# Kernel optimization log

Hardware: AMD Instinct MI355X
Metric: run time of the kernel (lower is better)

The kernel has to match this reference:

```python
import jax, jax.numpy as jnp
import numpy as np

DIM = 512
HEADS = 8
DIM_HEAD = 64
INNER = HEADS * DIM_HEAD
EPS = 1e-5


def setup_inputs() -> dict:
    key = jax.random.key(0)
    ks = jax.random.split(key, 8)
    x = jax.random.normal(ks[0], (4, 2048, DIM), dtype=jnp.float32)
    gamma = jnp.ones((DIM,), jnp.float32)
    beta = jnp.zeros((DIM,), jnp.float32)
    Wq = jax.random.normal(ks[1], (DIM, INNER), jnp.float32) / np.sqrt(DIM)
    Wkv = jax.random.normal(ks[2], (DIM, 2 * INNER), jnp.float32) / np.sqrt(DIM)
    mix_pre = jax.random.normal(ks[3], (HEADS, HEADS), jnp.float32)
    mix_post = jax.random.normal(ks[4], (HEADS, HEADS), jnp.float32)
    Wout = jax.random.normal(ks[5], (INNER, DIM), jnp.float32) / np.sqrt(INNER)
    bout = jnp.zeros((DIM,), jnp.float32)
    return {"x": x, "gamma": gamma, "beta": beta, "Wq": Wq, "Wkv": Wkv,
            "mix_pre": mix_pre, "mix_post": mix_post, "Wout": Wout, "bout": bout}


def reference(x, gamma, beta, Wq, Wkv, mix_pre, mix_post, Wout, bout):
    b, n, _ = x.shape
    scale = DIM_HEAD ** -0.5
    # LayerNorm
    mu = jnp.mean(x, axis=-1, keepdims=True)
    var = jnp.mean(jnp.square(x - mu), axis=-1, keepdims=True)
    xn = (x - mu) / jnp.sqrt(var + EPS) * gamma + beta
    # projections -> (b, h, n, d)
    q = (xn @ Wq).reshape(b, n, HEADS, DIM_HEAD).transpose(0, 2, 1, 3)
    kv = xn @ Wkv
    k, v = jnp.split(kv, 2, axis=-1)
    k = k.reshape(b, n, HEADS, DIM_HEAD).transpose(0, 2, 1, 3)
    v = v.reshape(b, n, HEADS, DIM_HEAD).transpose(0, 2, 1, 3)
    # talking-heads attention
    dots = jnp.einsum('bhid,bhjd->bhij', q, k) * scale
    dots = jnp.einsum('bhij,hg->bgij', dots, mix_pre)
    attn = jax.nn.softmax(dots, axis=-1)
    attn = jnp.einsum('bhij,hg->bgij', attn, mix_post)
    out = jnp.einsum('bhij,bhjd->bhid', attn, v)  # (b,h,n,d)
    out = out.transpose(0, 2, 1, 3).reshape(b, n, INNER)
    return out @ Wout + bout
```

## Files before the change

### kernel.cpp

```cpp
#include <hip/hip_runtime.h>

using short8  = short     __attribute__((ext_vector_type(8)));
using half4   = _Float16  __attribute__((ext_vector_type(4)));
using float4_ = float     __attribute__((ext_vector_type(4)));

__device__ __forceinline__ unsigned short f2bf(float f) {
  union { float f; unsigned u; } v; v.f = f;
  unsigned r = v.u + 0x7fffu + ((v.u >> 16) & 1u);
  return (unsigned short)(r >> 16);
}

__global__ __launch_bounds__(256, 4) void ln_kernel(
    const float* __restrict__ x, const float* __restrict__ gamma,
    const float* __restrict__ beta, unsigned short* __restrict__ xn) {
  int w = threadIdx.x >> 6, lane = threadIdx.x & 63;
  int row = blockIdx.x * 4 + w;
  const float4_* xr = (const float4_*)(x + row * 512);
  float4_ v0 = xr[lane * 2], v1 = xr[lane * 2 + 1];
  float s = 0.f, ss = 0.f;
#pragma unroll
  for (int e = 0; e < 4; ++e) { s += v0[e] + v1[e]; ss += v0[e]*v0[e] + v1[e]*v1[e]; }
#pragma unroll
  for (int off = 1; off < 64; off <<= 1) { s += __shfl_xor(s, off); ss += __shfl_xor(ss, off); }
  float mu = s * (1.f/512.f);
  float var = ss * (1.f/512.f) - mu*mu;
  float rs = rsqrtf(var + 1e-5f);
  const float4_* gp = (const float4_*)gamma;
  const float4_* bp = (const float4_*)beta;
  float4_ g0 = gp[lane*2], g1 = gp[lane*2+1], b0 = bp[lane*2], b1 = bp[lane*2+1];
  short8 pk;
#pragma unroll
  for (int e = 0; e < 4; ++e) {
    pk[e]   = (short)f2bf((v0[e]-mu)*rs*g0[e] + b0[e]);
    pk[e+4] = (short)f2bf((v1[e]-mu)*rs*g1[e] + b1[e]);
  }
  *(short8*)&xn[row*512 + lane*8] = pk;
}

__global__ __launch_bounds__(256, 4) void wconv(
    const float* __restrict__ Wq, const float* __restrict__ Wkv,
    const float* __restrict__ Wout, unsigned short* __restrict__ wt,
    unsigned short* __restrict__ wot) {
  int t = blockIdx.x * 256 + threadIdx.x;
  if (t < 786432) {
    int k = t / 1536, n = t % 1536;
    float v = (n < 512) ? Wq[k*512 + n] * 0.125f : Wkv[k*1024 + (n - 512)];
    wt[n*512 + k] = f2bf(v);
  } else {
    int t2 = t - 786432;
    int k = t2 >> 9, n = t2 & 511;
    wot[n*512 + k] = f2bf(Wout[k*512 + n]);
  }
}

__global__ __launch_bounds__(256, 2) void qkv_gemm(
    const unsigned short* __restrict__ A, const unsigned short* __restrict__ Bt,
    unsigned short* __restrict__ Qs, unsigned short* __restrict__ Kb,
    _Float16* __restrict__ Vt) {
  __shared__ unsigned short lA[128*32];
  __shared__ unsigned short lB[128*32];
  int bid = blockIdx.x;
  int tm = bid & 63, tn = bid >> 6;
  int m0 = tm * 128, n0 = tn * 128;
  int tid = threadIdx.x, lane = tid & 63, w = tid >> 6;
  int lrow = lane & 15, lgrp = lane >> 4;
  int wr = w >> 1, wc = w & 1;
  int r0 = tid >> 2, c0 = tid & 3;
  float4_ acc[4][4];
#pragma unroll
  for (int mi = 0; mi < 4; ++mi)
#pragma unroll
    for (int ni = 0; ni < 4; ++ni) acc[mi][ni] = (float4_){0.f,0.f,0.f,0.f};

  for (int k0 = 0; k0 < 512; k0 += 32) {
    short8 a0 = *(const short8*)&A[(m0 + r0)*512 + k0 + c0*8];
    short8 a1 = *(const short8*)&A[(m0 + 64 + r0)*512 + k0 + c0*8];
    short8 b0 = *(const short8*)&Bt[(n0 + r0)*512 + k0 + c0*8];
    short8 b1 = *(const short8*)&Bt[(n0 + 64 + r0)*512 + k0 + c0*8];
    __syncthreads();
    *(short8*)&lA[tid*8] = a0; *(short8*)&lA[(tid+256)*8] = a1;
    *(short8*)&lB[tid*8] = b0; *(short8*)&lB[(tid+256)*8] = b1;
    __syncthreads();
    short8 af[4], bfr[4];
#pragma unroll
    for (int mi = 0; mi < 4; ++mi) af[mi]  = *(const short8*)&lA[(wr*64 + mi*16 + lrow)*32 + lgrp*8];
#pragma unroll
    for (int ni = 0; ni < 4; ++ni) bfr[ni] = *(const short8*)&lB[(wc*64 + ni*16 + lrow)*32 + lgrp*8];
#pragma unroll
    for (int mi = 0; mi < 4; ++mi)
#pragma unroll
      for (int ni = 0; ni < 4; ++ni)
        acc[mi][ni] = __builtin_amdgcn_mfma_f32_16x16x32_bf16(af[mi], bfr[ni], acc[mi][ni], 0, 0, 0);
  }
#pragma unroll
  for (int mi = 0; mi < 4; ++mi) {
#pragma unroll
    for (int ni = 0; ni < 4; ++ni) {
      int col = n0 + wc*64 + ni*16 + lrow;
#pragma unroll
      for (int r = 0; r < 4; ++r) {
        int row = m0 + wr*64 + mi*16 + lgrp*4 + r;
        float v = acc[mi][ni][r];
        int b = row >> 11, i = row & 2047;
        if (col < 1024) {
          unsigned short* dst = (col < 512) ? Qs : Kb;
          int c = col & 511;
          dst[(((b<<3) + (c>>6))*2048 + i)*64 + (c & 63)] = f2bf(v);
        } else {
          int c = col - 1024;
          Vt[(((b<<3) + (c>>6))*64 + (c & 63))*2048 + i] = (_Float16)v;
        }
      }
    }
  }
}

__global__ __launch_bounds__(256, 1) void attn_kernel(
    const unsigned short* __restrict__ Qs, const unsigned short* __restrict__ Kb,
    const _Float16* __restrict__ Vt, const float* __restrict__ mixp,
    const float* __restrict__ mixq, unsigned short* __restrict__ AO) {
  int bid = blockIdx.x;
  int xcd = bid & 7;
  int b = xcd >> 1;
  int it = ((xcd & 1) << 6) | (bid >> 3);
  int i0 = it << 4;
  int tid = threadIdx.x, w = tid >> 6, lane = tid & 63;
  int lrow = lane & 15, lgrp = lane >> 4;

  __shared__ float Lm[4][8][16];
  __shared__ float Ll[4][8][16];
  __shared__ float Ob[8][64][16];

  short8 qf[8][2];
#pragma unroll
  for (int h = 0; h < 8; ++h) {
    int base = (((b<<3)+h)*2048 + i0 + lrow)*64 + lgrp*8;
#pragma unroll
    for (int t = 0; t < 2; ++t) qf[h][t] = *(const short8*)&Qs[base + t*32];
  }

  float m_[8], l_[8];
#pragma unroll
  for (int g = 0; g < 8; ++g) { m_[g] = -1e30f; l_[g] = 0.f; }

  for (int jt = w; jt < 128; jt += 4) {
    int j0 = jt << 4;
    short8 kfr[8][2];
#pragma unroll
    for (int h = 0; h < 8; ++h) {
      int base = (((b<<3)+h)*2048 + j0 + lrow)*64 + lgrp*8;
      kfr[h][0] = *(const short8*)&Kb[base];
      kfr[h][1] = *(const short8*)&Kb[base + 32];
    }
    float4_ S[8];
#pragma unroll
    for (int h = 0; h < 8; ++h) {
      float4_ z = {0.f,0.f,0.f,0.f};
      z = __builtin_amdgcn_mfma_f32_16x16x32_bf16(kfr[h][0], qf[h][0], z, 0, 0, 0);
      S[h] = __builtin_amdgcn_mfma_f32_16x16x32_bf16(kfr[h][1], qf[h][1], z, 0, 0, 0);
    }
#pragma unroll
    for (int g = 0; g < 8; ++g) {
      float4_ sg = S[0] * mixp[g];
#pragma unroll
      for (int h = 1; h < 8; ++h) sg += S[h] * mixp[h*8 + g];
      float tm = fmaxf(fmaxf(sg[0], sg[1]), fmaxf(sg[2], sg[3]));
      float mn = fmaxf(m_[g], tm);
      l_[g] = l_[g]*__expf(m_[g]-mn) + __expf(sg[0]-mn) + __expf(sg[1]-mn)
            + __expf(sg[2]-mn) + __expf(sg[3]-mn);
      m_[g] = mn;
    }
  }
#pragma unroll
  for (int g = 0; g < 8; ++g) {
#pragma unroll
    for (int off = 16; off < 64; off <<= 1) {
      float om = __shfl_xor(m_[g], off);
      float ol = __shfl_xor(l_[g], off);
      float mn = fmaxf(m_[g], om);
      l_[g] = l_[g]*__expf(m_[g]-mn) + ol*__expf(om-mn);
      m_[g] = mn;
    }
  }
  if (lgrp == 0) {
#pragma unroll
    for (int g = 0; g < 8; ++g) { Lm[w][g][lrow] = m_[g]; Ll[w][g][lrow] = l_[g]; }
  }
  __syncthreads();
  float mm[8];
#pragma unroll
  for (int g = 0; g < 8; ++g) {
    float M = Lm[0][g][lrow], L = Ll[0][g][lrow];
#pragma unroll
    for (int wv = 1; wv < 4; ++wv) {
      float om = Lm[wv][g][lrow], ol = Ll[wv][g][lrow];
      float mn = fmaxf(M, om);
      L = L*__expf(M-mn) + ol*__expf(om-mn);
      M = mn;
    }
    mm[g] = M + __logf(L);
  }

  float4_ ot[8][4];
#pragma unroll
  for (int g = 0; g < 8; ++g)
#pragma unroll
    for (int dt = 0; dt < 4; ++dt) ot[g][dt] = (float4_){0.f,0.f,0.f,0.f};

  for (int jt = w; jt < 128; jt += 4) {
    int j0 = jt << 4;
    short8 kfr[8][2];
#pragma unroll
    for (int h = 0; h < 8; ++h) {
      int base = (((b<<3)+h)*2048 + j0 + lrow)*64 + lgrp*8;
      kfr[h][0] = *(const short8*)&Kb[base];
      kfr[h][1] = *(const short8*)&Kb[base + 32];
    }
    float4_ S[8];
#pragma unroll
    for (int h = 0; h < 8; ++h) {
      float4_ z = {0.f,0.f,0.f,0.f};
      z = __builtin_amdgcn_mfma_f32_16x16x32_bf16(kfr[h][0], qf[h][0], z, 0, 0, 0);
      S[h] = __builtin_amdgcn_mfma_f32_16x16x32_bf16(kfr[h][1], qf[h][1], z, 0, 0, 0);
    }
    half4 vf[8][4];
#pragma unroll
    for (int g = 0; g < 8; ++g) {
      int vbase = ((((b<<3)+g)<<6) + lrow)*2048 + j0 + lgrp*4;
#pragma unroll
      for (int dt = 0; dt < 4; ++dt) vf[g][dt] = *(const half4*)&Vt[vbase + dt*16*2048];
    }
    float4_ P[8];
#pragma unroll
    for (int g = 0; g < 8; ++g) {
      float4_ sg = S[0] * mixp[g];
#pragma unroll
      for (int h = 1; h < 8; ++h) sg += S[h] * mixp[h*8 + g];
      float4_ p;
      p[0] = __expf(sg[0] - mm[g]); p[1] = __expf(sg[1] - mm[g]);
      p[2] = __expf(sg[2] - mm[g]); p[3] = __expf(sg[3] - mm[g]);
      P[g] = p;
    }
#pragma unroll
    for (int g = 0; g < 8; ++g) {
      float4_ ag = P[0] * mixq[g];
#pragma unroll
      for (int h = 1; h < 8; ++h) ag += P[h] * mixq[h*8 + g];
      half4 pb;
      pb[0] = (_Float16)ag[0]; pb[1] = (_Float16)ag[1];
      pb[2] = (_Float16)ag[2]; pb[3] = (_Float16)ag[3];
#pragma unroll
      for (int dt = 0; dt < 4; ++dt)
        ot[g][dt] = __builtin_amdgcn_mfma_f32_16x16x16f16(vf[g][dt], pb, ot[g][dt], 0, 0, 0);
    }
  }

#pragma unroll
  for (int wv = 0; wv < 4; ++wv) {
    if (w == wv) {
#pragma unroll
      for (int g = 0; g < 8; ++g)
#pragma unroll
        for (int dt = 0; dt < 4; ++dt)
#pragma unroll
          for (int r = 0; r < 4; ++r) {
            int d = dt*16 + lgrp*4 + r;
            if (wv == 0) Ob[g][d][lrow] = ot[g][dt][r];
            else         Ob[g][d][lrow] += ot[g][dt][r];
          }
    }
    __syncthreads();
  }
  int i = tid >> 4;
  int gd0 = (tid & 15) * 32;
  unsigned short* dst = &AO[(b*2048 + i0 + i)*512 + gd0];
  const float* ob = (const float*)Ob;
#pragma unroll
  for (int c = 0; c < 32; c += 8) {
    short8 pk;
#pragma unroll
    for (int e = 0; e < 8; ++e) pk[e] = (short)f2bf(ob[(gd0 + c + e)*16 + i]);
    *(short8*)&dst[c] = pk;
  }
}

__global__ __launch_bounds__(256, 2) void out_gemm(
    const unsigned short* __restrict__ A, const unsigned short* __restrict__ Bt,
    const float* __restrict__ bout, float* __restrict__ out) {
  __shared__ unsigned short lA[128*32];
  __shared__ unsigned short lB[128*32];
  int bid = blockIdx.x;
  int tm = bid & 63, tn = bid >> 6;
  int m0 = tm * 128, n0 = tn * 128;
  int tid = threadIdx.x, lane = tid & 63, w = tid >> 6;
  int lrow = lane & 15, lgrp = lane >> 4;
  int wr = w >> 1, wc = w & 1;
  int r0 = tid >> 2, c0 = tid & 3;
  float4_ acc[4][4];
#pragma unroll
  for (int mi = 0; mi < 4; ++mi)
#pragma unroll
    for (int ni = 0; ni < 4; ++ni) acc[mi][ni] = (float4_){0.f,0.f,0.f,0.f};

  for (int k0 = 0; k0 < 512; k0 += 32) {
    short8 a0 = *(const short8*)&A[(m0 + r0)*512 + k0 + c0*8];
    short8 a1 = *(const short8*)&A[(m0 + 64 + r0)*512 + k0 + c0*8];
    short8 b0 = *(const short8*)&Bt[(n0 + r0)*512 + k0 + c0*8];
    short8 b1 = *(const short8*)&Bt[(n0 + 64 + r0)*512 + k0 + c0*8];
    __syncthreads();
    *(short8*)&lA[tid*8] = a0; *(short8*)&lA[(tid+256)*8] = a1;
    *(short8*)&lB[tid*8] = b0; *(short8*)&lB[(tid+256)*8] = b1;
    __syncthreads();
    short8 af[4], bfr[4];
#pragma unroll
    for (int mi = 0; mi < 4; ++mi) af[mi]  = *(const short8*)&lA[(wr*64 + mi*16 + lrow)*32 + lgrp*8];
#pragma unroll
    for (int ni = 0; ni < 4; ++ni) bfr[ni] = *(const short8*)&lB[(wc*64 + ni*16 + lrow)*32 + lgrp*8];
#pragma unroll
    for (int mi = 0; mi < 4; ++mi)
#pragma unroll
      for (int ni = 0; ni < 4; ++ni)
        acc[mi][ni] = __builtin_amdgcn_mfma_f32_16x16x32_bf16(af[mi], bfr[ni], acc[mi][ni], 0, 0, 0);
  }
#pragma unroll
  for (int mi = 0; mi < 4; ++mi)
#pragma unroll
    for (int ni = 0; ni < 4; ++ni) {
      int col = n0 + wc*64 + ni*16 + lrow;
      float bb = bout[col];
#pragma unroll
      for (int r = 0; r < 4; ++r) {
        int row = m0 + wr*64 + mi*16 + lgrp*4 + r;
        out[row*512 + col] = acc[mi][ni][r] + bb;
      }
    }
}

extern "C" void kernel_launch(void* const* d_in, const int* in_sizes, int n_in,
                              void* d_out, int out_size, void* d_ws, size_t ws_size,
                              hipStream_t stream) {
  (void)in_sizes; (void)n_in; (void)out_size; (void)ws_size;
  const float* x     = (const float*)d_in[0];
  const float* gamma = (const float*)d_in[1];
  const float* beta  = (const float*)d_in[2];
  const float* Wq    = (const float*)d_in[3];
  const float* Wkv   = (const float*)d_in[4];
  const float* mixp  = (const float*)d_in[5];
  const float* mixq  = (const float*)d_in[6];
  const float* Wout  = (const float*)d_in[7];
  const float* bout  = (const float*)d_in[8];
  float* out = (float*)d_out;

  unsigned short* xn  = (unsigned short*)d_ws;
  unsigned short* wt  = xn  + 4194304;
  unsigned short* wot = wt  + 786432;
  unsigned short* Qs  = wot + 262144;
  unsigned short* Kb  = Qs  + 4194304;
  _Float16*       Vt  = (_Float16*)(Kb + 4194304);
  unsigned short* AO  = (unsigned short*)(Vt + 4194304);

  ln_kernel<<<2048, 256, 0, stream>>>(x, gamma, beta, xn);
  wconv<<<4096, 256, 0, stream>>>(Wq, Wkv, Wout, wt, wot);
  qkv_gemm<<<768, 256, 0, stream>>>(xn, wt, Qs, Kb, Vt);
  attn_kernel<<<512, 256, 0, stream>>>(Qs, Kb, Vt, mixp, mixq, AO);
  out_gemm<<<256, 256, 0, stream>>>(AO, wot, bout, out);
}
```

Measured before the change: 610.0 us.

## Split talking-heads attention into stats, merge and output kernels

The single attention kernel becomes three kernels. A stats pass splits the key range in two across blocks, a small kernel merges the partial max/sum, and an output pass splits the post-mix output heads in half across blocks. This gives 1024 blocks instead of 512 with higher occupancy, and the mixing coefficients are held in scalar registers. The post-softmax mix now runs in packed fp16, and Q is staged through LDS. In exchange, the output pass recomputes all eight QK head products for each half of the heads, adds an extra launch and intermediate buffers, and does the mix arithmetic at lower precision.

```diff
diff --git a/kernel.cpp b/kernel.cpp
--- a/kernel.cpp
+++ b/kernel.cpp
@@ -1,13 +1,21 @@
 #include <hip/hip_runtime.h>
 
 using short8  = short     __attribute__((ext_vector_type(8)));
+using half2v  = _Float16  __attribute__((ext_vector_type(2)));
 using half4   = _Float16  __attribute__((ext_vector_type(4)));
+using float2_ = float     __attribute__((ext_vector_type(2)));
 using float4_ = float     __attribute__((ext_vector_type(4)));
 
 __device__ __forceinline__ unsigned short f2bf(float f) {
   union { float f; unsigned u; } v; v.f = f;
   unsigned r = v.u + 0x7fffu + ((v.u >> 16) & 1u);
   return (unsigned short)(r >> 16);
+}
+__device__ __forceinline__ float sgprf(float x) {
+  return __int_as_float(__builtin_amdgcn_readfirstlane(__float_as_int(x)));
+}
+__device__ __forceinline__ half2v pkrtz(float a, float b) {
+  return __builtin_bit_cast(half2v, __builtin_amdgcn_cvt_pkrtz(a, b));
 }
 
 __global__ __launch_bounds__(256, 4) void ln_kernel(
@@ -39,17 +47,25 @@
 
 __global__ __launch_bounds__(256, 4) void wconv(
     const float* __restrict__ Wq, const float* __restrict__ Wkv,
-    const float* __restrict__ Wout, unsigned short* __restrict__ wt,
-    unsigned short* __restrict__ wot) {
+    const float* __restrict__ Wout, const float* __restrict__ mixq,
+    unsigned short* __restrict__ wt, unsigned short* __restrict__ wot,
+    unsigned int* __restrict__ mqp) {
   int t = blockIdx.x * 256 + threadIdx.x;
   if (t < 786432) {
     int k = t / 1536, n = t % 1536;
     float v = (n < 512) ? Wq[k*512 + n] * 0.125f : Wkv[k*1024 + (n - 512)];
     wt[n*512 + k] = f2bf(v);
-  } else {
+  } else if (t < 1048576) {
     int t2 = t - 786432;
     int k = t2 >> 9, n = t2 & 511;
     wot[n*512 + k] = f2bf(Wout[k*512 + n]);
+  } else if (t < 1048608) {
+    int idx = t - 1048576;
+    int gp = idx >> 2, p = idx & 3;
+    _Float16 lo = (_Float16)mixq[gp*8 + 2*p];
+    _Float16 hi = (_Float16)mixq[gp*8 + 2*p + 1];
+    unsigned short lb = *(unsigned short*)&lo, hb = *(unsigned short*)&hi;
+    mqp[idx] = (unsigned)lb | ((unsigned)hb << 16);
   }
 }
 
@@ -115,59 +131,76 @@
   }
 }
 
-__global__ __launch_bounds__(256, 1) void attn_kernel(
+__device__ __forceinline__ void stage_q(const unsigned short* __restrict__ Qs,
+                                        unsigned short* qlds, int b, int i0, int tid) {
+#pragma unroll
+  for (int q = 0; q < 4; ++q) {
+    int idx = q*256 + tid;
+    int h = idx >> 7, i = (idx >> 3) & 15, c = idx & 7;
+    short8 v = *(const short8*)&Qs[(((b<<3)+h)*2048 + i0 + i)*64 + c*8];
+    *(short8*)&qlds[((h*8 + c)*16 + i)*8] = v;
+  }
+}
+
+__global__ __launch_bounds__(256, 4) void attn1(
     const unsigned short* __restrict__ Qs, const unsigned short* __restrict__ Kb,
-    const _Float16* __restrict__ Vt, const float* __restrict__ mixp,
-    const float* __restrict__ mixq, unsigned short* __restrict__ AO) {
+    const float* __restrict__ mixp, float* __restrict__ ml) {
+  __shared__ unsigned short qlds[8192];
+  __shared__ float Lm[4][8][16], Ll[4][8][16];
   int bid = blockIdx.x;
-  int xcd = bid & 7;
-  int b = xcd >> 1;
-  int it = ((xcd & 1) << 6) | (bid >> 3);
+  int xcd = bid & 7, b = xcd >> 1, jh = xcd & 1, it = bid >> 3;
   int i0 = it << 4;
   int tid = threadIdx.x, w = tid >> 6, lane = tid & 63;
   int lrow = lane & 15, lgrp = lane >> 4;
 
-  __shared__ float Lm[4][8][16];
-  __shared__ float Ll[4][8][16];
-  __shared__ float Ob[8][64][16];
-
-  short8 qf[8][2];
-#pragma unroll
-  for (int h = 0; h < 8; ++h) {
-    int base = (((b<<3)+h)*2048 + i0 + lrow)*64 + lgrp*8;
-#pragma unroll
-    for (int t = 0; t < 2; ++t) qf[h][t] = *(const short8*)&Qs[base + t*32];
-  }
+  float mp[64];
+#pragma unroll
+  for (int k = 0; k < 64; ++k) mp[k] = sgprf(mixp[k]);
+
+  stage_q(Qs, qlds, b, i0, tid);
+  __syncthreads();
 
   float m_[8], l_[8];
 #pragma unroll
   for (int g = 0; g < 8; ++g) { m_[g] = -1e30f; l_[g] = 0.f; }
 
-  for (int jt = w; jt < 128; jt += 4) {
+  for (int t = 0; t < 16; ++t) {
+    int jt = (jh << 6) + w + (t << 2);
     int j0 = jt << 4;
-    short8 kfr[8][2];
-#pragma unroll
-    for (int h = 0; h < 8; ++h) {
-      int base = (((b<<3)+h)*2048 + j0 + lrow)*64 + lgrp*8;
-      kfr[h][0] = *(const short8*)&Kb[base];
-      kfr[h][1] = *(const short8*)&Kb[base + 32];
-    }
     float4_ S[8];
 #pragma unroll
-    for (int h = 0; h < 8; ++h) {
-      float4_ z = {0.f,0.f,0.f,0.f};
-      z = __builtin_amdgcn_mfma_f32_16x16x32_bf16(kfr[h][0], qf[h][0], z, 0, 0, 0);
-      S[h] = __builtin_amdgcn_mfma_f32_16x16x32_bf16(kfr[h][1], qf[h][1], z, 0, 0, 0);
+    for (int hb = 0; hb < 2; ++hb) {
+      short8 kf[4][2];
+#pragma unroll
+      for (int hh = 0; hh < 4; ++hh) {
+        const unsigned short* kp = &Kb[(((b<<3)+hb*4+hh)*2048 + j0 + lrow)*64 + lgrp*8];
+        kf[hh][0] = *(const short8*)kp;
+        kf[hh][1] = *(const short8*)(kp + 32);
+      }
+#pragma unroll
+      for (int hh = 0; hh < 4; ++hh) {
+        int h = hb*4 + hh;
+        short8 q0 = *(const short8*)&qlds[((h*8 + lgrp)*16 + lrow)*8];
+        short8 q1 = *(const short8*)&qlds[((h*8 + lgrp + 4)*16 + lrow)*8];
+        float4_ z = {0.f,0.f,0.f,0.f};
+        z = __builtin_amdgcn_mfma_f32_16x16x32_bf16(kf[hh][0], q0, z, 0, 0, 0);
+        S[h] = __builtin_amdgcn_mfma_f32_16x16x32_bf16(kf[hh][1], q1, z, 0, 0, 0);
+      }
     }
 #pragma unroll
     for (int g = 0; g < 8; ++g) {
-      float4_ sg = S[0] * mixp[g];
-#pragma unroll
-      for (int h = 1; h < 8; ++h) sg += S[h] * mixp[h*8 + g];
-      float tm = fmaxf(fmaxf(sg[0], sg[1]), fmaxf(sg[2], sg[3]));
+      float2_ sa = (float2_){S[0][0], S[0][1]} * mp[g];
+      float2_ sb = (float2_){S[0][2], S[0][3]} * mp[g];
+#pragma unroll
+      for (int h = 1; h < 8; ++h) {
+        float m = mp[h*8 + g];
+        sa += (float2_){S[h][0], S[h][1]} * m;
+        sb += (float2_){S[h][2], S[h][3]} * m;
+      }
+      float tm = fmaxf(fmaxf(sa[0], sa[1]), fmaxf(sb[0], sb[1]));
       float mn = fmaxf(m_[g], tm);
-      l_[g] = l_[g]*__expf(m_[g]-mn) + __expf(sg[0]-mn) + __expf(sg[1]-mn)
-            + __expf(sg[2]-mn) + __expf(sg[3]-mn);
+      l_[g] = l_[g]*__expf(m_[g]-mn) + __expf(sa[0]-mn) + __expf(sa[1]-mn)
+            + __expf(sb[0]-mn) + __expf(sb[1]-mn);
       m_[g] = mn;
     }
   }
@@ -187,79 +220,139 @@
     for (int g = 0; g < 8; ++g) { Lm[w][g][lrow] = m_[g]; Ll[w][g][lrow] = l_[g]; }
   }
   __syncthreads();
-  float mm[8];
-#pragma unroll
-  for (int g = 0; g < 8; ++g) {
-    float M = Lm[0][g][lrow], L = Ll[0][g][lrow];
-#pragma unroll
-    for (int wv = 1; wv < 4; ++wv) {
-      float om = Lm[wv][g][lrow], ol = Ll[wv][g][lrow];
-      float mn = fmaxf(M, om);
-      L = L*__expf(M-mn) + ol*__expf(om-mn);
-      M = mn;
-    }
-    mm[g] = M + __logf(L);
-  }
-
-  float4_ ot[8][4];
-#pragma unroll
-  for (int g = 0; g < 8; ++g)
+  if (w == 0 && lgrp == 0) {
+    int gi = b*2048 + i0 + lrow;
+#pragma unroll
+    for (int g = 0; g < 8; ++g) {
+      float M = Lm[0][g][lrow], L = Ll[0][g][lrow];
+#pragma unroll
+      for (int wv = 1; wv < 4; ++wv) {
+        float om = Lm[wv][g][lrow], ol = Ll[wv][g][lrow];
+        float mn = fmaxf(M, om);
+        L = L*__expf(M-mn) + ol*__expf(om-mn); M = mn;
+      }
+      ml[((jh*8192 + gi)*8 + g)*2]     = M;
+      ml[((jh*8192 + gi)*8 + g)*2 + 1] = L;
+    }
+  }
+}
+
+__global__ __launch_bounds__(256, 8) void attn1m(const float* __restrict__ ml,
+                                                 float* __restrict__ mm) {
+  int idx = blockIdx.x*256 + threadIdx.x;
+  float m0 = ml[idx*2], l0 = ml[idx*2+1];
+  float m1 = ml[(65536+idx)*2], l1 = ml[(65536+idx)*2+1];
+  float M = fmaxf(m0, m1);
+  float L = l0*__expf(m0-M) + l1*__expf(m1-M);
+  mm[idx] = M + __logf(L);
+}
+
+__global__ __launch_bounds__(256, 3) void attn2(
+    const unsigned short* __restrict__ Qs, const unsigned short* __restrict__ Kb,
+    const _Float16* __restrict__ Vt, const float* __restrict__ mixp,
+    const unsigned int* __restrict__ mqp, const float* __restrict__ mm,
+    unsigned short* __restrict__ AO) {
+  __shared__ unsigned short qlds[8192];
+  __shared__ float Ob[4][64][16];
+  int bid = blockIdx.x;
+  int xcd = bid & 7, b = xcd >> 1, gh = xcd & 1, it = bid >> 3;
+  int i0 = it << 4;
+  int tid = threadIdx.x, w = tid >> 6, lane = tid & 63;
+  int lrow = lane & 15, lgrp = lane >> 4;
+
+  float mp[64];
+#pragma unroll
+  for (int k = 0; k < 64; ++k) mp[k] = sgprf(mixp[k]);
+  half2v mq2[8][2];
+#pragma unroll
+  for (int gp = 0; gp < 8; ++gp)
+#pragma unroll
+    for (int p = 0; p < 2; ++p) {
+      unsigned u = mqp[gp*4 + gh*2 + p];
+      mq2[gp][p] = __builtin_bit_cast(half2v, u);
+    }
+
+  stage_q(Qs, qlds, b, i0, tid);
+  float mmr[8];
+  int gi = b*2048 + i0 + lrow;
+#pragma unroll
+  for (int g = 0; g < 8; ++g) mmr[g] = mm[gi*8 + g];
+  __syncthreads();
+
+  float4_ ot[4][4];
+#pragma unroll
+  for (int g = 0; g < 4; ++g)
 #pragma unroll
     for (int dt = 0; dt < 4; ++dt) ot[g][dt] = (float4_){0.f,0.f,0.f,0.f};
 
-  for (int jt = w; jt < 128; jt += 4) {
+  for (int t = 0; t < 32; ++t) {
+    int jt = w + (t << 2);
     int j0 = jt << 4;
-    short8 kfr[8][2];
-#pragma unroll
-    for (int h = 0; h < 8; ++h) {
-      int base = (((b<<3)+h)*2048 + j0 + lrow)*64 + lgrp*8;
-      kfr[h][0] = *(const short8*)&Kb[base];
-      kfr[h][1] = *(const short8*)&Kb[base + 32];
-    }
     float4_ S[8];
 #pragma unroll
-    for (int h = 0; h < 8; ++h) {
-      float4_ z = {0.f,0.f,0.f,0.f};
-      z = __builtin_amdgcn_mfma_f32_16x16x32_bf16(kfr[h][0], qf[h][0], z, 0, 0, 0);
-      S[h] = __builtin_amdgcn_mfma_f32_16x16x32_bf16(kfr[h][1], qf[h][1], z, 0, 0, 0);
-    }
-    half4 vf[8][4];
+    for (int hb = 0; hb < 4; ++hb) {
+      short8 kf[2][2];
+#pragma unroll
+      for (int hh = 0; hh < 2; ++hh) {
+        const unsigned short* kp = &Kb[(((b<<3)+hb*2+hh)*2048 + j0 + lrow)*64 + lgrp*8];
+        kf[hh][0] = *(const short8*)kp;
+        kf[hh][1] = *(const short8*)(kp + 32);
+      }
+#pragma unroll
+      for (int hh = 0; hh < 2; ++hh) {
+        int h = hb*2 + hh;
+        short8 q0 = *(const short8*)&qlds[((h*8 + lgrp)*16 + lrow)*8];
+        short8 q1 = *(const short8*)&qlds[((h*8 + lgrp + 4)*16 + lrow)*8];
+        float4_ z = {0.f,0.f,0.f,0.f};
+        z = __builtin_amdgcn_mfma_f32_16x16x32_bf16(kf[hh][0], q0, z, 0, 0, 0);
+        S[h] = __builtin_amdgcn_mfma_f32_16x16x32_bf16(kf[hh][1], q1, z, 0, 0, 0);
+      }
+    }
+    half2v agv[4][2];
+#pragma unroll
+    for (int r = 0; r < 4; ++r) { agv[r][0] = (half2v)0; agv[r][1] = (half2v)0; }
 #pragma unroll
     for (int g = 0; g < 8; ++g) {
-      int vbase = ((((b<<3)+g)<<6) + lrow)*2048 + j0 + lgrp*4;
-#pragma unroll
-      for (int dt = 0; dt < 4; ++dt) vf[g][dt] = *(const half4*)&Vt[vbase + dt*16*2048];
-    }
-    float4_ P[8];
-#pragma unroll
-    for (int g = 0; g < 8; ++g) {
-      float4_ sg = S[0] * mixp[g];
-#pragma unroll
-      for (int h = 1; h < 8; ++h) sg += S[h] * mixp[h*8 + g];
-      float4_ p;
-      p[0] = __expf(sg[0] - mm[g]); p[1] = __expf(sg[1] - mm[g]);
-      p[2] = __expf(sg[2] - mm[g]); p[3] = __expf(sg[3] - mm[g]);
-      P[g] = p;
-    }
-#pragma unroll
-    for (int g = 0; g < 8; ++g) {
-      float4_ ag = P[0] * mixq[g];
-#pragma unroll
-      for (int h = 1; h < 8; ++h) ag += P[h] * mixq[h*8 + g];
-      half4 pb;
-      pb[0] = (_Float16)ag[0]; pb[1] = (_Float16)ag[1];
-      pb[2] = (_Float16)ag[2]; pb[3] = (_Float16)ag[3];
-#pragma unroll
-      for (int dt = 0; dt < 4; ++dt)
-        ot[g][dt] = __builtin_amdgcn_mfma_f32_16x16x16f16(vf[g][dt], pb, ot[g][dt], 0, 0, 0);
-    }
-  }
-
+      float2_ sa = (float2_){S[0][0], S[0][1]} * mp[g];
+      float2_ sb = (float2_){S[0][2], S[0][3]} * mp[g];
+#pragma unroll
+      for (int h = 1; h < 8; ++h) {
+        float m = mp[h*8 + g];
+        sa += (float2_){S[h][0], S[h][1]} * m;
+        sb += (float2_){S[h][2], S[h][3]} * m;
+      }
+      float p0 = __expf(sa[0]-mmr[g]), p1 = __expf(sa[1]-mmr[g]);
+      float p2 = __expf(sb[0]-mmr[g]), p3 = __expf(sb[1]-mmr[g]);
+      half2v d0 = pkrtz(p0, p0);
+      half2v d1 = pkrtz(p1, p1);
+      half2v d2 = pkrtz(p2, p2);
+      half2v d3 = pkrtz(p3, p3);
+      agv[0][0] += d0*mq2[g][0]; agv[0][1] += d0*mq2[g][1];
+      agv[1][0] += d1*mq2[g][0]; agv[1][1] += d1*mq2[g][1];
+      agv[2][0] += d2*mq2[g][0]; agv[2][1] += d2*mq2[g][1];
+      agv[3][0] += d3*mq2[g][0]; agv[3][1] += d3*mq2[g][1];
+    }
+    half4 pb[4];
+#pragma unroll
+    for (int g = 0; g < 4; ++g) {
+#pragma unroll
+      for (int r = 0; r < 4; ++r) pb[g][r] = agv[r][g >> 1][g & 1];
+    }
+#pragma unroll
+    for (int g = 0; g < 4; ++g) {
+      const _Float16* vb = &Vt[(((b<<3) + gh*4 + g)*64 + lrow)*2048 + j0 + lgrp*4];
+#pragma unroll
+      for (int dt = 0; dt < 4; ++dt) {
+        half4 vf = *(const half4*)&vb[dt*16*2048];
+        ot[g][dt] = __builtin_amdgcn_mfma_f32_16x16x16f16(vf, pb[g], ot[g][dt], 0, 0, 0);
+      }
+    }
+  }
 #pragma unroll
   for (int wv = 0; wv < 4; ++wv) {
     if (w == wv) {
 #pragma unroll
-      for (int g = 0; g < 8; ++g)
+      for (int g = 0; g < 4; ++g)
 #pragma unroll
         for (int dt = 0; dt < 4; ++dt)
 #pragma unroll
@@ -271,17 +364,18 @@
     }
     __syncthreads();
   }
-  int i = tid >> 4;
-  int gd0 = (tid & 15) * 32;
-  unsigned short* dst = &AO[(b*2048 + i0 + i)*512 + gd0];
-  const float* ob = (const float*)Ob;
-#pragma unroll
-  for (int c = 0; c < 32; c += 8) {
-    short8 pk;
-#pragma unroll
-    for (int e = 0; e < 8; ++e) pk[e] = (short)f2bf(ob[(gd0 + c + e)*16 + i]);
-    *(short8*)&dst[c] = pk;
-  }
+  int i = tid >> 4, cc = tid & 15;
+  unsigned short* dst = &AO[(b*2048 + i0 + i)*512 + gh*256 + cc*16];
+  short8 o0, o1;
+#pragma unroll
+  for (int e = 0; e < 8; ++e) {
+    int c = cc*16 + e;
+    o0[e] = (short)f2bf(Ob[c>>6][c&63][i]);
+    int c2 = c + 8;
+    o1[e] = (short)f2bf(Ob[c2>>6][c2&63][i]);
+  }
+  *(short8*)dst = o0;
+  *(short8*)(dst + 8) = o1;
 }
 
 __global__ __launch_bounds__(256, 2) void out_gemm(
@@ -358,10 +452,15 @@
   unsigned short* Kb  = Qs  + 4194304;
   _Float16*       Vt  = (_Float16*)(Kb + 4194304);
   unsigned short* AO  = (unsigned short*)(Vt + 4194304);
+  unsigned int*   mqp = (unsigned int*)(AO + 4194304);
+  float*          ml  = (float*)(mqp + 32);
+  float*          mm  = ml + 262144;
 
   ln_kernel<<<2048, 256, 0, stream>>>(x, gamma, beta, xn);
-  wconv<<<4096, 256, 0, stream>>>(Wq, Wkv, Wout, wt, wot);
+  wconv<<<4097, 256, 0, stream>>>(Wq, Wkv, Wout, mixq, wt, wot, mqp);
   qkv_gemm<<<768, 256, 0, stream>>>(xn, wt, Qs, Kb, Vt);
-  attn_kernel<<<512, 256, 0, stream>>>(Qs, Kb, Vt, mixp, mixq, AO);
+  attn1<<<1024, 256, 0, stream>>>(Qs, Kb, mixp, ml);
+  attn1m<<<256, 256, 0, stream>>>(ml, mm);
+  attn2<<<1024, 256, 0, stream>>>(Qs, Kb, Vt, mixp, mqp, mm, AO);
   out_gemm<<<256, 256, 0, stream>>>(AO, wot, bout, out);
 }
```

Result: slower. 1.038 ms (+70.1%).

## Split attention work per head across waves with LDS exchange for head mixing

Applied to the files above, without the earlier changes.

The attention kernel now uses 512 threads, one wave per head, instead of 4 waves that each handle all 8 heads over a strided slice of key tiles. Each wave computes QK for its own head over every key tile and writes fp16-packed scores to a double-buffered LDS array. After a barrier, every wave reads all heads' scores to apply the pre-softmax mix, and in the second pass the post-softmax mix, using packed half2 arithmetic. K loads are software-pipelined one tile ahead, and the cross-wave Ob reduction and merge of softmax statistics are removed. In exchange there are one or two block barriers per key tile, and scores and probabilities are rounded to fp16 (round-toward-zero) before mixing, which lowers accuracy.

```diff
diff --git a/kernel.cpp b/kernel.cpp
--- a/kernel.cpp
+++ b/kernel.cpp
@@ -1,13 +1,25 @@
 #include <hip/hip_runtime.h>
 
+using short4_ = short     __attribute__((ext_vector_type(4)));
 using short8  = short     __attribute__((ext_vector_type(8)));
+using half2v  = _Float16  __attribute__((ext_vector_type(2)));
 using half4   = _Float16  __attribute__((ext_vector_type(4)));
+using float2_ = float     __attribute__((ext_vector_type(2)));
 using float4_ = float     __attribute__((ext_vector_type(4)));
 
 __device__ __forceinline__ unsigned short f2bf(float f) {
   union { float f; unsigned u; } v; v.f = f;
   unsigned r = v.u + 0x7fffu + ((v.u >> 16) & 1u);
   return (unsigned short)(r >> 16);
+}
+__device__ __forceinline__ float sgprf(float x) {
+  return __int_as_float(__builtin_amdgcn_readfirstlane(__float_as_int(x)));
+}
+__device__ __forceinline__ half2v pkrtz(float a, float b) {
+  return __builtin_bit_cast(half2v, __builtin_amdgcn_cvt_pkrtz(a, b));
+}
+__device__ __forceinline__ void bar_lds() {
+  asm volatile("s_waitcnt lgkmcnt(0)\ns_barrier" ::: "memory");
 }
 
 __global__ __launch_bounds__(256, 4) void ln_kernel(
@@ -39,8 +51,8 @@
 
 __global__ __launch_bounds__(256, 4) void wconv(
     const float* __restrict__ Wq, const float* __restrict__ Wkv,
-    const float* __restrict__ Wout, unsigned short* __restrict__ wt,
-    unsigned short* __restrict__ wot) {
+    const float* __restrict__ Wout,
+    unsigned short* __restrict__ wt, unsigned short* __restrict__ wot) {
   int t = blockIdx.x * 256 + threadIdx.x;
   if (t < 786432) {
     int k = t / 1536, n = t % 1536;
@@ -115,172 +127,149 @@
   }
 }
 
-__global__ __launch_bounds__(256, 1) void attn_kernel(
+__global__ __launch_bounds__(512, 4) void attn_f(
     const unsigned short* __restrict__ Qs, const unsigned short* __restrict__ Kb,
     const _Float16* __restrict__ Vt, const float* __restrict__ mixp,
     const float* __restrict__ mixq, unsigned short* __restrict__ AO) {
+  __shared__ unsigned long long sbuf[2][8][64];
+  __shared__ unsigned long long pbuf[2][8][64];
   int bid = blockIdx.x;
-  int xcd = bid & 7;
-  int b = xcd >> 1;
-  int it = ((xcd & 1) << 6) | (bid >> 3);
+  int b = (bid & 7) >> 1;
+  int it = ((bid >> 3) << 1) | (bid & 1);
   int i0 = it << 4;
   int tid = threadIdx.x, w = tid >> 6, lane = tid & 63;
   int lrow = lane & 15, lgrp = lane >> 4;
-
-  __shared__ float Lm[4][8][16];
-  __shared__ float Ll[4][8][16];
-  __shared__ float Ob[8][64][16];
-
-  short8 qf[8][2];
-#pragma unroll
-  for (int h = 0; h < 8; ++h) {
-    int base = (((b<<3)+h)*2048 + i0 + lrow)*64 + lgrp*8;
-#pragma unroll
-    for (int t = 0; t < 2; ++t) qf[h][t] = *(const short8*)&Qs[base + t*32];
-  }
-
-  float m_[8], l_[8];
-#pragma unroll
-  for (int g = 0; g < 8; ++g) { m_[g] = -1e30f; l_[g] = 0.f; }
-
-  for (int jt = w; jt < 128; jt += 4) {
-    int j0 = jt << 4;
-    short8 kfr[8][2];
+  int bh = (b << 3) + w;
+
+  float mp[8];
+#pragma unroll
+  for (int h = 0; h < 8; ++h) mp[h] = sgprf(mixp[h*8 + w]);
+  unsigned mqs[8];
+#pragma unroll
+  for (int g = 0; g < 8; ++g) {
+    float v = mixq[g*8 + w];
+    half2v h2 = pkrtz(v, v);
+    mqs[g] = (unsigned)__builtin_amdgcn_readfirstlane((int)__builtin_bit_cast(unsigned, h2));
+  }
+
+  const unsigned short* qp = &Qs[(bh*2048 + i0 + lrow)*64 + lgrp*8];
+  short8 qf0 = *(const short8*)qp;
+  short8 qf1 = *(const short8*)(qp + 32);
+
+  const unsigned short* kbase = &Kb[(bh*2048 + lrow)*64 + lgrp*8];
+  const _Float16*       vbase = &Vt[(bh*64 + lrow)*2048 + lgrp*4];
+
+  short8 ka0 = *(const short8*)kbase;
+  short8 ka1 = *(const short8*)(kbase + 32);
+  short8 kb0, kb1;
+
+  float m_ = -1e30f, l_ = 0.f;
+
+  auto p1body = [&](int t, short8& c0, short8& c1, short8& n0, short8& n1) {
+    const unsigned short* kn = kbase + (((t + 1) & 127) << 10);
+    n0 = *(const short8*)kn;
+    n1 = *(const short8*)(kn + 32);
+    float4_ S = {0.f,0.f,0.f,0.f};
+    S = __builtin_amdgcn_mfma_f32_16x16x32_bf16(c0, qf0, S, 0, 0, 0);
+    S = __builtin_amdgcn_mfma_f32_16x16x32_bf16(c1, qf1, S, 0, 0, 0);
+    unsigned lo = __builtin_bit_cast(unsigned, pkrtz(S[0], S[1]));
+    unsigned hi = __builtin_bit_cast(unsigned, pkrtz(S[2], S[3]));
+    sbuf[t & 1][w][lane] = (unsigned long long)lo | ((unsigned long long)hi << 32);
+    bar_lds();
+    float s0 = 0.f, s1 = 0.f, s2 = 0.f, s3 = 0.f;
 #pragma unroll
     for (int h = 0; h < 8; ++h) {
-      int base = (((b<<3)+h)*2048 + j0 + lrow)*64 + lgrp*8;
-      kfr[h][0] = *(const short8*)&Kb[base];
-      kfr[h][1] = *(const short8*)&Kb[base + 32];
-    }
-    float4_ S[8];
+      unsigned long long u = sbuf[t & 1][h][lane];
+      half2v l2 = __builtin_bit_cast(half2v, (unsigned)u);
+      half2v h2 = __builtin_bit_cast(half2v, (unsigned)(u >> 32));
+      s0 = fmaf(mp[h], (float)l2[0], s0);
+      s1 = fmaf(mp[h], (float)l2[1], s1);
+      s2 = fmaf(mp[h], (float)h2[0], s2);
+      s3 = fmaf(mp[h], (float)h2[1], s3);
+    }
+    float tm = fmaxf(fmaxf(s0, s1), fmaxf(s2, s3));
+    float mn = fmaxf(m_, tm);
+    l_ = l_*__expf(m_-mn) + __expf(s0-mn) + __expf(s1-mn) + __expf(s2-mn) + __expf(s3-mn);
+    m_ = mn;
+  };
+  for (int tt = 0; tt < 64; ++tt) {
+    p1body(2*tt,     ka0, ka1, kb0, kb1);
+    p1body(2*tt + 1, kb0, kb1, ka0, ka1);
+  }
+#pragma unroll
+  for (int off = 16; off < 64; off <<= 1) {
+    float om = __shfl_xor(m_, off);
+    float ol = __shfl_xor(l_, off);
+    float mn = fmaxf(m_, om);
+    l_ = l_*__expf(m_-mn) + ol*__expf(om-mn);
+    m_ = mn;
+  }
+  float mm = m_ + __logf(l_);
+
+  float4_ ot0 = {0.f,0.f,0.f,0.f}, ot1 = ot0, ot2 = ot0, ot3 = ot0;
+  auto p2body = [&](int t, short8& c0, short8& c1, short8& n0, short8& n1) {
+    const unsigned short* kn = kbase + (((t + 1) & 127) << 10);
+    n0 = *(const short8*)kn;
+    n1 = *(const short8*)(kn + 32);
+    const _Float16* vb = vbase + (t << 4);
+    half4 vf0 = *(const half4*)vb;
+    half4 vf1 = *(const half4*)(vb + 16*2048);
+    half4 vf2 = *(const half4*)(vb + 32*2048);
+    half4 vf3 = *(const half4*)(vb + 48*2048);
+    float4_ S = {0.f,0.f,0.f,0.f};
+    S = __builtin_amdgcn_mfma_f32_16x16x32_bf16(c0, qf0, S, 0, 0, 0);
+    S = __builtin_amdgcn_mfma_f32_16x16x32_bf16(c1, qf1, S, 0, 0, 0);
+    unsigned lo = __builtin_bit_cast(unsigned, pkrtz(S[0], S[1]));
+    unsigned hi = __builtin_bit_cast(unsigned, pkrtz(S[2], S[3]));
+    sbuf[t & 1][w][lane] = (unsigned long long)lo | ((unsigned long long)hi << 32);
+    bar_lds();
+    float s0 = 0.f, s1 = 0.f, s2 = 0.f, s3 = 0.f;
 #pragma unroll
     for (int h = 0; h < 8; ++h) {
-      float4_ z = {0.f,0.f,0.f,0.f};
-      z = __builtin_amdgcn_mfma_f32_16x16x32_bf16(kfr[h][0], qf[h][0], z, 0, 0, 0);
-      S[h] = __builtin_amdgcn_mfma_f32_16x16x32_bf16(kfr[h][1], qf[h][1], z, 0, 0, 0);
-    }
+      unsigned long long u = sbuf[t & 1][h][lane];
+      half2v l2 = __builtin_bit_cast(half2v, (unsigned)u);
+      half2v h2 = __builtin_bit_cast(half2v, (unsigned)(u >> 32));
+      s0 = fmaf(mp[h], (float)l2[0], s0);
+      s1 = fmaf(mp[h], (float)l2[1], s1);
+      s2 = fmaf(mp[h], (float)h2[0], s2);
+      s3 = fmaf(mp[h], (float)h2[1], s3);
+    }
+    float p0 = __expf(s0 - mm), p1 = __expf(s1 - mm);
+    float p2 = __expf(s2 - mm), p3 = __expf(s3 - mm);
+    unsigned plo = __builtin_bit_cast(unsigned, pkrtz(p0, p1));
+    unsigned phi = __builtin_bit_cast(unsigned, pkrtz(p2, p3));
+    pbuf[t & 1][w][lane] = (unsigned long long)plo | ((unsigned long long)phi << 32);
+    bar_lds();
+    half2v A0 = (half2v)0, A1 = (half2v)0;
 #pragma unroll
     for (int g = 0; g < 8; ++g) {
-      float4_ sg = S[0] * mixp[g];
-#pragma unroll
-      for (int h = 1; h < 8; ++h) sg += S[h] * mixp[h*8 + g];
-      float tm = fmaxf(fmaxf(sg[0], sg[1]), fmaxf(sg[2], sg[3]));
-      float mn = fmaxf(m_[g], tm);
-      l_[g] = l_[g]*__expf(m_[g]-mn) + __expf(sg[0]-mn) + __expf(sg[1]-mn)
-            + __expf(sg[2]-mn) + __expf(sg[3]-mn);
-      m_[g] = mn;
-    }
-  }
-#pragma unroll
-  for (int g = 0; g < 8; ++g) {
-#pragma unroll
-    for (int off = 16; off < 64; off <<= 1) {
-      float om = __shfl_xor(m_[g], off);
-      float ol = __shfl_xor(l_[g], off);
-      float mn = fmaxf(m_[g], om);
-      l_[g] = l_[g]*__expf(m_[g]-mn) + ol*__expf(om-mn);
-      m_[g] = mn;
-    }
-  }
-  if (lgrp == 0) {
-#pragma unroll
-    for (int g = 0; g < 8; ++g) { Lm[w][g][lrow] = m_[g]; Ll[w][g][lrow] = l_[g]; }
-  }
-  __syncthreads();
-  float mm[8];
-#pragma unroll
-  for (int g = 0; g < 8; ++g) {
-    float M = Lm[0][g][lrow], L = Ll[0][g][lrow];
-#pragma unroll
-    for (int wv = 1; wv < 4; ++wv) {
-      float om = Lm[wv][g][lrow], ol = Ll[wv][g][lrow];
-      float mn = fmaxf(M, om);
-      L = L*__expf(M-mn) + ol*__expf(om-mn);
-      M = mn;
-    }
-    mm[g] = M + __logf(L);
-  }
-
-  float4_ ot[8][4];
-#pragma unroll
-  for (int g = 0; g < 8; ++g)
-#pragma unroll
-    for (int dt = 0; dt < 4; ++dt) ot[g][dt] = (float4_){0.f,0.f,0.f,0.f};
-
-  for (int jt = w; jt < 128; jt += 4) {
-    int j0 = jt << 4;
-    short8 kfr[8][2];
-#pragma unroll
-    for (int h = 0; h < 8; ++h) {
-      int base = (((b<<3)+h)*2048 + j0 + lrow)*64 + lgrp*8;
-      kfr[h][0] = *(const short8*)&Kb[base];
-      kfr[h][1] = *(const short8*)&Kb[base + 32];
-    }
-    float4_ S[8];
-#pragma unroll
-    for (int h = 0; h < 8; ++h) {
-      float4_ z = {0.f,0.f,0.f,0.f};
-      z = __builtin_amdgcn_mfma_f32_16x16x32_bf16(kfr[h][0], qf[h][0], z, 0, 0, 0);
-      S[h] = __builtin_amdgcn_mfma_f32_16x16x32_bf16(kfr[h][1], qf[h][1], z, 0, 0, 0);
-    }
-    half4 vf[8][4];
-#pragma unroll
-    for (int g = 0; g < 8; ++g) {
-      int vbase = ((((b<<3)+g)<<6) + lrow)*2048 + j0 + lgrp*4;
-#pragma unroll
-      for (int dt = 0; dt < 4; ++dt) vf[g][dt] = *(const half4*)&Vt[vbase + dt*16*2048];
-    }
-    float4_ P[8];
-#pragma unroll
-    for (int g = 0; g < 8; ++g) {
-      float4_ sg = S[0] * mixp[g];
-#pragma unroll
-      for (int h = 1; h < 8; ++h) sg += S[h] * mixp[h*8 + g];
-      float4_ p;
-      p[0] = __expf(sg[0] - mm[g]); p[1] = __expf(sg[1] - mm[g]);
-      p[2] = __expf(sg[2] - mm[g]); p[3] = __expf(sg[3] - mm[g]);
-      P[g] = p;
-    }
-#pragma unroll
-    for (int g = 0; g < 8; ++g) {
-      float4_ ag = P[0] * mixq[g];
-#pragma unroll
-      for (int h = 1; h < 8; ++h) ag += P[h] * mixq[h*8 + g];
-      half4 pb;
-      pb[0] = (_Float16)ag[0]; pb[1] = (_Float16)ag[1];
-      pb[2] = (_Float16)ag[2]; pb[3] = (_Float16)ag[3];
-#pragma unroll
-      for (int dt = 0; dt < 4; ++dt)
-        ot[g][dt] = __builtin_amdgcn_mfma_f32_16x16x16f16(vf[g][dt], pb, ot[g][dt], 0, 0, 0);
-    }
-  }
-
-#pragma unroll
-  for (int wv = 0; wv < 4; ++wv) {
-    if (w == wv) {
-#pragma unroll
-      for (int g = 0; g < 8; ++g)
-#pragma unroll
-        for (int dt = 0; dt < 4; ++dt)
-#pragma unroll
-          for (int r = 0; r < 4; ++r) {
-            int d = dt*16 + lgrp*4 + r;
-            if (wv == 0) Ob[g][d][lrow] = ot[g][dt][r];
-            else         Ob[g][d][lrow] += ot[g][dt][r];
-          }
-    }
-    __syncthreads();
-  }
-  int i = tid >> 4;
-  int gd0 = (tid & 15) * 32;
-  unsigned short* dst = &AO[(b*2048 + i0 + i)*512 + gd0];
-  const float* ob = (const float*)Ob;
-#pragma unroll
-  for (int c = 0; c < 32; c += 8) {
-    short8 pk;
-#pragma unroll
-    for (int e = 0; e < 8; ++e) pk[e] = (short)f2bf(ob[(gd0 + c + e)*16 + i]);
-    *(short8*)&dst[c] = pk;
+      unsigned long long u = pbuf[t & 1][g][lane];
+      half2v l2 = __builtin_bit_cast(half2v, (unsigned)u);
+      half2v h2 = __builtin_bit_cast(half2v, (unsigned)(u >> 32));
+      half2v m2 = __builtin_bit_cast(half2v, mqs[g]);
+      A0 += m2 * l2;
+      A1 += m2 * h2;
+    }
+    half4 pb;
+    pb[0] = A0[0]; pb[1] = A0[1]; pb[2] = A1[0]; pb[3] = A1[1];
+    ot0 = __builtin_amdgcn_mfma_f32_16x16x16f16(vf0, pb, ot0, 0, 0, 0);
+    ot1 = __builtin_amdgcn_mfma_f32_16x16x16f16(vf1, pb, ot1, 0, 0, 0);
+    ot2 = __builtin_amdgcn_mfma_f32_16x16x16f16(vf2, pb, ot2, 0, 0, 0);
+    ot3 = __builtin_amdgcn_mfma_f32_16x16x16f16(vf3, pb, ot3, 0, 0, 0);
+  };
+  for (int tt = 0; tt < 64; ++tt) {
+    p2body(2*tt,     ka0, ka1, kb0, kb1);
+    p2body(2*tt + 1, kb0, kb1, ka0, ka1);
+  }
+
+  unsigned short* ao = &AO[(b*2048 + i0 + lrow)*512 + w*64 + lgrp*4];
+  float4_ ov[4] = {ot0, ot1, ot2, ot3};
+#pragma unroll
+  for (int dt = 0; dt < 4; ++dt) {
+    short4_ pk;
+#pragma unroll
+    for (int r = 0; r < 4; ++r) pk[r] = (short)f2bf(ov[dt][r]);
+    *(short4_*)(ao + dt*16) = pk;
   }
 }
 
@@ -362,6 +351,6 @@
   ln_kernel<<<2048, 256, 0, stream>>>(x, gamma, beta, xn);
   wconv<<<4096, 256, 0, stream>>>(Wq, Wkv, Wout, wt, wot);
   qkv_gemm<<<768, 256, 0, stream>>>(xn, wt, Qs, Kb, Vt);
-  attn_kernel<<<512, 256, 0, stream>>>(Qs, Kb, Vt, mixp, mixq, AO);
+  attn_f<<<512, 512, 0, stream>>>(Qs, Kb, Vt, mixp, mixq, AO);
   out_gemm<<<256, 256, 0, stream>>>(AO, wot, bout, out);
 }
```

Result: faster. 580.8 us (-4.8%).
